# Kernel optimization log

Hardware: AMD Instinct MI355X
Metric: run time of the kernel (lower is better)

Reference implementation:

```python
import jax, jax.numpy as jnp
import numpy as np

TIME = 10  # interpolation factor, hardcoded in the torch module


def _interpolation(poly, time=TIME):
    # poly: [B, M, 2] -> [B, M*time, 2]
    poly_roll = jnp.roll(poly, shift=1, axis=1)
    step = jnp.arange(time, dtype=poly.dtype) / time  # [time]
    # interp[b, m, t, c] = poly[b,m,c]*step[t] + roll[b,m,c]*(1-step[t])
    interp = (poly[:, :, None, :] * step[None, None, :, None]
              + poly_roll[:, :, None, :] * (1.0 - step)[None, None, :, None])
    B, M = poly.shape[0], poly.shape[1]
    return interp.reshape(B, M * time, 2)


def _compute_distance(pred_poly, gt_poly):
    # pred: [B, N, 2], gt: [B, G, 2] -> sq dist [B, G, N]
    diff = pred_poly[:, None, :, :] - gt_poly[:, :, None, :]
    return jnp.sum(diff * diff, axis=3)


def setup_inputs() -> dict:
    key = jax.random.key(0)
    k1, k2, k3 = jax.random.split(key, 3)
    B, N, M = 1024, 128, 128
    return {
        "ini_pred_poly": jax.random.normal(k1, (B, N, 2), dtype=jnp.float32),
        "pred_polys_": jax.random.normal(k2, (B, N, 2), dtype=jnp.float32),
        "gt_polys": jax.random.normal(k3, (B, M, 2), dtype=jnp.float32),
        "keyPointsMask": jnp.ones((B, M), dtype=jnp.float32),
    }


def reference(ini_pred_poly, pred_polys_, gt_polys, keyPointsMask):
    # ---- lossPred2NearestGt ----
    gt_interp = _interpolation(gt_polys)                     # [B, M*T, 2]
    dist_pg = _compute_distance(ini_pred_poly, gt_interp)    # [B, M*T, N]
    index_gt = jnp.argmin(dist_pg, axis=1)                   # [B, N]
    nearest_gt = jnp.take_along_axis(gt_interp, index_gt[:, :, None], axis=1)  # [B, N, 2]
    loss_pred2gt = jnp.mean(jnp.abs(pred_polys_ - nearest_gt))  # l1, mean reduction

    # ---- lossGt2NearestPred ----
    dist_gp = _compute_distance(ini_pred_poly, gt_polys)     # [B, M, N]
    index_pred = jnp.argmin(dist_gp, axis=2)                 # [B, M]
    nearest_pred = jnp.take_along_axis(pred_polys_, index_pred[:, :, None], axis=1)  # [B, M, 2]
    loss_gt2pred = jnp.abs(nearest_pred - gt_polys)          # [B, M, 2], reduction='none'

    mask = keyPointsMask[:, :, None] * jnp.ones((1, 1, 2), dtype=keyPointsMask.dtype)  # [B, M, 2]
    loss_set2set = jnp.sum(loss_gt2pred * mask) / (jnp.sum(mask) + 1.0) + loss_pred2gt
    return loss_set2set / 2.0
```

## Files before the change

### kernel.cpp

```cpp
#include <hip/hip_runtime.h>

constexpr int Bn = 1024;
constexpr int Nn = 128;
constexpr int Mn = 128;


__global__ __launch_bounds__(256) void dm_main(
    const float2* __restrict__ ini,
    const float2* __restrict__ pred,
    const float2* __restrict__ gt,
    const float*  __restrict__ kpm,
    float4* __restrict__ part)
{
    __shared__ float4 s_segA[Mn];
    __shared__ float2 s_segB[Mn];
    __shared__ float2 s_ini[Nn];
    __shared__ float2 s_pred[Nn];
    __shared__ float2 s_gt[Mn];
    __shared__ float  s_red[3][4];

    const int b   = blockIdx.x;
    const int tid = threadIdx.x;

    if (tid < Mn) {
        const float2 cur = gt[b*Mn + tid];
        const float2 prv = gt[b*Mn + ((tid + Mn - 1) & (Mn - 1))];
        const float ex = cur.x - prv.x, ey = cur.y - prv.y;
        const float ee = fmaxf(fmaf(ex, ex, ey*ey), 1e-30f);
        const float nr = -10.0f * __builtin_amdgcn_rcpf(ee);
        s_segA[tid] = make_float4(prv.x, prv.y, ex, ey);
        s_segB[tid] = make_float2(ee, nr);
        s_gt[tid]   = cur;
        s_ini[tid]  = ini[b*Nn + tid];
        s_pred[tid] = pred[b*Nn + tid];
    }
    __syncthreads();

    const int lane_s = tid & 1;
    const int n      = tid >> 1;
    const int base   = lane_s * 64;

    const float2 p = s_ini[n];
    float best = 3.4e38f; int bm = 0; float bs = 0.f;
    #pragma unroll 8
    for (int i = 0; i < 64; ++i) {
        const int m = base + i;
        const float4 A  = s_segA[m];
        const float2 Bv = s_segB[m];
        const float fx = A.x - p.x, fy = A.y - p.y;
        const float fe = fmaf(fx, A.z, fy*A.w);
        const float ff = fmaf(fx, fx, fy*fy);
        float tv = fe * Bv.y;
        tv = fminf(fmaxf(rintf(tv), 0.f), 9.f);
        const float sp = tv * 0.1f;
        const float d  = fmaf(sp, fmaf(sp, Bv.x, fe + fe), ff);
        if (d < best) { best = d; bm = m; bs = sp; }
    }
    {
        const float od = __shfl_xor(best, 1);
        const int   om = __shfl_xor(bm, 1);
        const float os = __shfl_xor(bs, 1);
        if (od < best || (od == best && om < bm)) { best = od; bm = om; bs = os; }
    }
    float sum_p2g = 0.f;
    if (lane_s == 0) {
        const float4 A = s_segA[bm];
        const float ngx = fmaf(bs, A.z, A.x);
        const float ngy = fmaf(bs, A.w, A.y);
        const float2 pr = s_pred[n];
        sum_p2g = fabsf(pr.x - ngx) + fabsf(pr.y - ngy);
    }

    const float2 g = s_gt[n];
    float best2 = 3.4e38f; int ni = 0;
    #pragma unroll 8
    for (int i = 0; i < 64; ++i) {
        const int j = base + i;
        const float2 q = s_ini[j];
        const float dx = q.x - g.x, dy = q.y - g.y;
        const float d = fmaf(dx, dx, dy*dy);
        if (d < best2) { best2 = d; ni = j; }
    }
    {
        const float od = __shfl_xor(best2, 1);
        const int   oi = __shfl_xor(ni, 1);
        if (od < best2 || (od == best2 && oi < ni)) { best2 = od; ni = oi; }
    }
    float sum_g2p = 0.f, sum_m = 0.f;
    if (lane_s == 0) {
        const float  w   = kpm[b*Mn + n];
        const float2 np_ = s_pred[ni];
        sum_g2p = w * (fabsf(np_.x - g.x) + fabsf(np_.y - g.y));
        sum_m   = 2.0f * w;
    }

    #pragma unroll
    for (int off = 32; off > 0; off >>= 1) {
        sum_p2g += __shfl_down(sum_p2g, off);
        sum_g2p += __shfl_down(sum_g2p, off);
        sum_m   += __shfl_down(sum_m,   off);
    }
    const int wv = tid >> 6;
    if ((tid & 63) == 0) { s_red[0][wv] = sum_p2g; s_red[1][wv] = sum_g2p; s_red[2][wv] = sum_m; }
    __syncthreads();
    if (tid == 0) {
        part[b] = make_float4(s_red[0][0] + s_red[0][1] + s_red[0][2] + s_red[0][3],
                              s_red[1][0] + s_red[1][1] + s_red[1][2] + s_red[1][3],
                              s_red[2][0] + s_red[2][1] + s_red[2][2] + s_red[2][3], 0.f);
    }
}

__global__ __launch_bounds__(1024) void dm_final(const float4* __restrict__ part,
                                                 float* __restrict__ out)
{
    __shared__ float s_red[3][16];
    const int tid = threadIdx.x;
    const float4 v = part[tid];
    float a = v.x, c = v.y, m = v.z;
    #pragma unroll
    for (int off = 32; off > 0; off >>= 1) {
        a += __shfl_down(a, off); c += __shfl_down(c, off); m += __shfl_down(m, off);
    }
    const int wv = tid >> 6;
    if ((tid & 63) == 0) { s_red[0][wv] = a; s_red[1][wv] = c; s_red[2][wv] = m; }
    __syncthreads();
    if (tid == 0) {
        float A = 0.f, C = 0.f, M = 0.f;
        #pragma unroll
        for (int i = 0; i < 16; ++i) { A += s_red[0][i]; C += s_red[1][i]; M += s_red[2][i]; }
        out[0] = (C / (M + 1.0f) + A * (1.0f / 262144.0f)) * 0.5f;
    }
}

extern "C" void kernel_launch(void* const* d_in, const int* in_sizes, int n_in,
                              void* d_out, int out_size, void* d_ws, size_t ws_size,
                              hipStream_t stream)
{
    const float2* ini  = (const float2*)d_in[0];
    const float2* pred = (const float2*)d_in[1];
    const float2* gt   = (const float2*)d_in[2];
    const float*  kpm  = (const float*)d_in[3];
    float*  out  = (float*)d_out;
    float4* part = (float4*)d_ws;

    dm_main<<<Bn, 256, 0, stream>>>(ini, pred, gt, kpm, part);
    dm_final<<<1, 1024, 0, stream>>>(part, out);
}
```

Baseline: 73.12 us.

## Register-block two query points per thread and split the segment range across waves

New measurement: 73.18 us. No clear change (+0.1%).

```diff
diff --git a/kernel.cpp b/kernel.cpp
--- a/kernel.cpp
+++ b/kernel.cpp
@@ -4,23 +4,29 @@
 constexpr int Nn = 128;
 constexpr int Mn = 128;
 
+__device__ float4 g_part[Bn];
+
 
 __global__ __launch_bounds__(256) void dm_main(
     const float2* __restrict__ ini,
     const float2* __restrict__ pred,
     const float2* __restrict__ gt,
-    const float*  __restrict__ kpm,
-    float4* __restrict__ part)
+    const float*  __restrict__ kpm)
 {
     __shared__ float4 s_segA[Mn];
     __shared__ float2 s_segB[Mn];
     __shared__ float2 s_ini[Nn];
     __shared__ float2 s_pred[Nn];
     __shared__ float2 s_gt[Mn];
+    __shared__ float4 s_cA[4][Nn];
+    __shared__ float2 s_cB[4][Mn];
     __shared__ float  s_red[3][4];
 
     const int b   = blockIdx.x;
     const int tid = threadIdx.x;
+
+    float kw = 0.f;
+    if (tid >= Nn) kw = kpm[b*Mn + (tid - Nn)];
 
     if (tid < Mn) {
         const float2 cur = gt[b*Mn + tid];
@@ -31,67 +37,98 @@
         s_segA[tid] = make_float4(prv.x, prv.y, ex, ey);
         s_segB[tid] = make_float2(ee, nr);
         s_gt[tid]   = cur;
-        s_ini[tid]  = ini[b*Nn + tid];
-        s_pred[tid] = pred[b*Nn + tid];
+    } else {
+        const int t = tid - Mn;
+        s_ini[t]  = ini[b*Nn + t];
+        s_pred[t] = pred[b*Nn + t];
     }
     __syncthreads();
 
-    const int lane_s = tid & 1;
-    const int n      = tid >> 1;
-    const int base   = lane_s * 64;
+    const int lane  = tid & 63;
+    const int w     = tid >> 6;
+    const int mbase = w * 32;
 
-    const float2 p = s_ini[n];
-    float best = 3.4e38f; int bm = 0; float bs = 0.f;
-    #pragma unroll 8
-    for (int i = 0; i < 64; ++i) {
-        const int m = base + i;
+    const float2 p0 = s_ini[lane];
+    const float2 p1 = s_ini[lane + 64];
+    const float2 g0 = s_gt[lane];
+    const float2 g1 = s_gt[lane + 64];
+
+    float bd0 = 3.4e38f, bd1 = 3.4e38f;
+    int   bm0 = 0,       bm1 = 0;
+    float bs0 = 0.f,     bs1 = 0.f;
+    float cd0 = 3.4e38f, cd1 = 3.4e38f;
+    int   cj0 = 0,       cj1 = 0;
+
+    #pragma unroll 4
+    for (int i = 0; i < 32; ++i) {
+        const int m = mbase + i;
         const float4 A  = s_segA[m];
         const float2 Bv = s_segB[m];
-        const float fx = A.x - p.x, fy = A.y - p.y;
-        const float fe = fmaf(fx, A.z, fy*A.w);
-        const float ff = fmaf(fx, fx, fy*fy);
-        float tv = fe * Bv.y;
-        tv = fminf(fmaxf(rintf(tv), 0.f), 9.f);
-        const float sp = tv * 0.1f;
-        const float d  = fmaf(sp, fmaf(sp, Bv.x, fe + fe), ff);
-        if (d < best) { best = d; bm = m; bs = sp; }
+        const float2 q  = s_ini[m];
+        {
+            const float fx = A.x - p0.x, fy = A.y - p0.y;
+            const float fe = fmaf(fx, A.z, fy*A.w);
+            const float ff = fmaf(fx, fx, fy*fy);
+            float tv = fe * Bv.y;
+            tv = fminf(fmaxf(rintf(tv), 0.f), 9.f);
+            const float sp = tv * 0.1f;
+            const float d  = fmaf(sp, fmaf(sp, Bv.x, fe + fe), ff);
+            if (d < bd0) { bd0 = d; bm0 = m; bs0 = sp; }
+        }
+        {
+            const float fx = A.x - p1.x, fy = A.y - p1.y;
+            const float fe = fmaf(fx, A.z, fy*A.w);
+            const float ff = fmaf(fx, fx, fy*fy);
+            float tv = fe * Bv.y;
+            tv = fminf(fmaxf(rintf(tv), 0.f), 9.f);
+            const float sp = tv * 0.1f;
+            const float d  = fmaf(sp, fmaf(sp, Bv.x, fe + fe), ff);
+            if (d < bd1) { bd1 = d; bm1 = m; bs1 = sp; }
+        }
+        {
+            const float dx = q.x - g0.x, dy = q.y - g0.y;
+            const float d = fmaf(dx, dx, dy*dy);
+            if (d < cd0) { cd0 = d; cj0 = m; }
+        }
+        {
+            const float dx = q.x - g1.x, dy = q.y - g1.y;
+            const float d = fmaf(dx, dx, dy*dy);
+            if (d < cd1) { cd1 = d; cj1 = m; }
+        }
     }
-    {
-        const float od = __shfl_xor(best, 1);
-        const int   om = __shfl_xor(bm, 1);
-        const float os = __shfl_xor(bs, 1);
-        if (od < best || (od == best && om < bm)) { best = od; bm = om; bs = os; }
-    }
-    float sum_p2g = 0.f;
-    if (lane_s == 0) {
+
+    s_cA[w][lane]      = make_float4(bd0, bs0, __int_as_float(bm0), 0.f);
+    s_cA[w][lane + 64] = make_float4(bd1, bs1, __int_as_float(bm1), 0.f);
+    s_cB[w][lane]      = make_float2(cd0, __int_as_float(cj0));
+    s_cB[w][lane + 64] = make_float2(cd1, __int_as_float(cj1));
+    __syncthreads();
+
+    float sum_p2g = 0.f, sum_g2p = 0.f, sum_m = 0.f;
+    if (tid < Nn) {
+        const int n = tid;
+        float best = 3.4e38f; float bs = 0.f; int bm = 0;
+        #pragma unroll
+        for (int w2 = 0; w2 < 4; ++w2) {
+            const float4 c = s_cA[w2][n];
+            if (c.x < best) { best = c.x; bs = c.y; bm = __float_as_int(c.z); }
+        }
         const float4 A = s_segA[bm];
         const float ngx = fmaf(bs, A.z, A.x);
         const float ngy = fmaf(bs, A.w, A.y);
         const float2 pr = s_pred[n];
         sum_p2g = fabsf(pr.x - ngx) + fabsf(pr.y - ngy);
-    }
-
-    const float2 g = s_gt[n];
-    float best2 = 3.4e38f; int ni = 0;
-    #pragma unroll 8
-    for (int i = 0; i < 64; ++i) {
-        const int j = base + i;
-        const float2 q = s_ini[j];
-        const float dx = q.x - g.x, dy = q.y - g.y;
-        const float d = fmaf(dx, dx, dy*dy);
-        if (d < best2) { best2 = d; ni = j; }
-    }
-    {
-        const float od = __shfl_xor(best2, 1);
-        const int   oi = __shfl_xor(ni, 1);
-        if (od < best2 || (od == best2 && oi < ni)) { best2 = od; ni = oi; }
-    }
-    float sum_g2p = 0.f, sum_m = 0.f;
-    if (lane_s == 0) {
-        const float  w   = kpm[b*Mn + n];
-        const float2 np_ = s_pred[ni];
-        sum_g2p = w * (fabsf(np_.x - g.x) + fabsf(np_.y - g.y));
-        sum_m   = 2.0f * w;
+    } else {
+        const int m = tid - Nn;
+        float best = 3.4e38f; int nj = 0;
+        #pragma unroll
+        for (int w2 = 0; w2 < 4; ++w2) {
+            const float2 c = s_cB[w2][m];
+            if (c.x < best) { best = c.x; nj = __float_as_int(c.y); }
+        }
+        const float2 np_ = s_pred[nj];
+        const float2 g   = s_gt[m];
+        sum_g2p = kw * (fabsf(np_.x - g.x) + fabsf(np_.y - g.y));
+        sum_m   = 2.0f * kw;
     }
 
     #pragma unroll
@@ -104,18 +141,17 @@
     if ((tid & 63) == 0) { s_red[0][wv] = sum_p2g; s_red[1][wv] = sum_g2p; s_red[2][wv] = sum_m; }
     __syncthreads();
     if (tid == 0) {
-        part[b] = make_float4(s_red[0][0] + s_red[0][1] + s_red[0][2] + s_red[0][3],
-                              s_red[1][0] + s_red[1][1] + s_red[1][2] + s_red[1][3],
-                              s_red[2][0] + s_red[2][1] + s_red[2][2] + s_red[2][3], 0.f);
+        g_part[b] = make_float4(s_red[0][0] + s_red[0][1] + s_red[0][2] + s_red[0][3],
+                                s_red[1][0] + s_red[1][1] + s_red[1][2] + s_red[1][3],
+                                s_red[2][0] + s_red[2][1] + s_red[2][2] + s_red[2][3], 0.f);
     }
 }
 
-__global__ __launch_bounds__(1024) void dm_final(const float4* __restrict__ part,
-                                                 float* __restrict__ out)
+__global__ __launch_bounds__(1024) void dm_final(float* __restrict__ out)
 {
     __shared__ float s_red[3][16];
     const int tid = threadIdx.x;
-    const float4 v = part[tid];
+    const float4 v = g_part[tid];
     float a = v.x, c = v.y, m = v.z;
     #pragma unroll
     for (int off = 32; off > 0; off >>= 1) {
@@ -140,9 +176,8 @@
     const float2* pred = (const float2*)d_in[1];
     const float2* gt   = (const float2*)d_in[2];
     const float*  kpm  = (const float*)d_in[3];
-    float*  out  = (float*)d_out;
-    float4* part = (float4*)d_ws;
+    float* out = (float*)d_out;
 
-    dm_main<<<Bn, 256, 0, stream>>>(ini, pred, gt, kpm, part);
-    dm_final<<<1, 1024, 0, stream>>>(part, out);
+    dm_main<<<Bn, 256, 0, stream>>>(ini, pred, gt, kpm);
+    dm_final<<<1, 1024, 0, stream>>>(out);
 }
```
